# Performance work log

Measured on AMD Instinct MI355X. Metric: run time of the kernel, lower is better.

## Reference

```python
import jax, jax.numpy as jnp
import numpy as np

A = 32           # num_atoms
R = A * (A - 1)  # num_rel (fully connected, no self loops)
B, T, D = 4, 64, 64
S, E = 4, 4      # num_states, edge_types
MH, MO, NH = 256, 256, 256

def _lrelu(x):
    return jax.nn.leaky_relu(x, 0.01)  # torch default slope

def setup_inputs() -> dict:
    key = jax.random.key(0)
    ks = jax.random.split(key, 16)
    # one-hot receiver/sender matrices for a fully connected graph
    off = np.ones((A, A)) - np.eye(A)
    rec_idx, send_idx = np.where(off)
    eye = np.eye(A, dtype=np.float32)
    rel_rec = jnp.asarray(eye[rec_idx])    # [R, A]
    rel_send = jnp.asarray(eye[send_idx])  # [R, A]
    w = 0.05
    return {
        "inputs": jax.random.normal(ks[0], (B, A, T, D), jnp.float32),
        "state": jax.random.uniform(ks[1], (B, A, T, S), jnp.float32),
        "rel_type": jax.random.uniform(ks[2], (B, R, S, E), jnp.float32),
        "rel_rec": rel_rec,
        "rel_send": rel_send,
        "msg_fc1_w": jax.random.normal(ks[3], (E, 2 * D, MH), jnp.float32) * w,
        "msg_fc1_b": jax.random.normal(ks[4], (E, MH), jnp.float32) * w,
        "msg_fc2_w": jax.random.normal(ks[5], (E, MH, MO), jnp.float32) * w,
        "msg_fc2_b": jax.random.normal(ks[6], (E, MO), jnp.float32) * w,
        "out_fc1_w": jax.random.normal(ks[7], (D + MO, NH), jnp.float32) * w,
        "out_fc1_b": jax.random.normal(ks[8], (NH,), jnp.float32) * w,
        "out_fc2_w": jax.random.normal(ks[9], (NH, NH), jnp.float32) * w,
        "out_fc2_b": jax.random.normal(ks[10], (NH,), jnp.float32) * w,
        "out_fc3_w": jax.random.normal(ks[11], (NH, D), jnp.float32) * w,
        "out_fc3_b": jax.random.normal(ks[12], (D,), jnp.float32) * w,
        "pred_steps": 1,
    }

def reference(inputs, state, rel_type, rel_rec, rel_send,
              msg_fc1_w, msg_fc1_b, msg_fc2_w, msg_fc2_b,
              out_fc1_w, out_fc1_b, out_fc2_w, out_fc2_b,
              out_fc3_w, out_fc3_b, pred_steps):
    # hidden_states=True, embedding=False, ball_pos=None, skip_first=True,
    # dropout p=0, pred_steps=1 -> one single_step_forward over all T.
    x = jnp.transpose(inputs, (0, 2, 1, 3))   # [B,T,A,D]
    st = jnp.transpose(state, (0, 2, 1, 3))   # [B,T,A,S]
    t = x.shape[1]

    # gather via one-hot matmuls
    recv = jnp.einsum('ra,btad->btrd', rel_rec, x)    # [B,T,R,D]
    send = jnp.einsum('ra,btad->btrd', rel_send, x)   # [B,T,R,D]
    ss = jnp.einsum('ra,btas->btrs', rel_send, st)    # [B,T,R,S]
    pre_msg = jnp.concatenate([send, recv], axis=-1)  # [B,T,R,2D]

    all_msgs = jnp.zeros(pre_msg.shape[:3] + (MO,), pre_msg.dtype)
    for i in range(1, E):  # skip_first_edge_type
        m = _lrelu(pre_msg @ msg_fc1_w[i] + msg_fc1_b[i])
        m = _lrelu(m @ msg_fc2_w[i] + msg_fc2_b[i])
        # gate: sum over states of rel_type[...,i] * sender states
        g = jnp.einsum('brs,btrs->btr', rel_type[..., i], ss)[..., None]
        all_msgs = all_msgs + m * g

    # scatter-accumulate messages back to receiver nodes
    agg = jnp.einsum('btrm,ra->btam', all_msgs, rel_rec)  # [B,T,A,MO]
    aug = jnp.concatenate([x, agg], axis=-1)              # skip_connection = inputs
    h = _lrelu(aug @ out_fc1_w + out_fc1_b)
    h = _lrelu(h @ out_fc2_w + out_fc2_b)
    pred = h @ out_fc3_w + out_fc3_b
    nxt = x + pred                                        # [B,T,A,D]

    out = nxt[:, : t - 1]                                 # pred_all
    return jnp.transpose(out, (0, 2, 1, 3))               # [B,A,T-1,D]
```

## Files before the change

### kernel.cpp

```cpp
#include <hip/hip_runtime.h>


typedef _Float16 f16x8 __attribute__((ext_vector_type(8)));
typedef float f32x4 __attribute__((ext_vector_type(4)));

#define MFMAH(a, b, c) __builtin_amdgcn_mfma_f32_16x16x32_f16((a), (b), (c), 0, 0, 0)

#define KBAR0() do {                                             \
  __builtin_amdgcn_sched_barrier(0);                             \
  asm volatile("s_waitcnt vmcnt(0) lgkmcnt(0)" ::: "memory");    \
  __builtin_amdgcn_s_barrier();                                  \
  __builtin_amdgcn_sched_barrier(0);                             \
} while (0)

#define KBARL() do {                                             \
  __builtin_amdgcn_sched_barrier(0);                             \
  asm volatile("s_waitcnt lgkmcnt(0)" ::: "memory");             \
  __builtin_amdgcn_s_barrier();                                  \
  __builtin_amdgcn_sched_barrier(0);                             \
} while (0)

__device__ __forceinline__ unsigned pkh(float lo, float hi) {
  auto h = __builtin_amdgcn_cvt_pkrtz(lo, hi);
  return __builtin_bit_cast(unsigned, h);
}
__device__ __forceinline__ unsigned short f2h(float f) {
  return __builtin_bit_cast(unsigned short, (_Float16)f);
}
__device__ __forceinline__ float lrelu(float x) { return x > 0.f ? x : 0.01f * x; }

__device__ __forceinline__ void gl16(const void* g, void* l) {
  __builtin_amdgcn_global_load_lds(
      (const __attribute__((address_space(1))) unsigned int*)(unsigned long long)g,
      (__attribute__((address_space(3))) unsigned int*)(unsigned int)(unsigned long long)l,
      16, 0, 0);
}

__global__ __launch_bounds__(256) void kw(
    const float* __restrict__ w1, const float* __restrict__ w2,
    const float* __restrict__ o1, const float* __restrict__ o2, const float* __restrict__ o3,
    unsigned short* __restrict__ W1T, unsigned short* __restrict__ W2F,
    unsigned short* __restrict__ O1T, unsigned short* __restrict__ O2T,
    unsigned short* __restrict__ O3T) {
  int i = blockIdx.x * 256 + threadIdx.x;
  if (i < 98304) {
    int k = i & 63, n = (i >> 6) & 255, eh = i >> 14;
    int e = (eh >> 1) + 1, half = eh & 1;
    W1T[i] = f2h(w1[(e * 128 + half * 64 + k) * 256 + n]);
    return;
  }
  i -= 98304;
  if (i < 196608) {
    int j = i & 7, l = (i >> 3) & 63, t = (i >> 9) & 15, s = (i >> 13) & 7, e = i >> 16;
    int n = t * 16 + (l & 15);
    int k = s * 32 + (l >> 4) * 8 + j;
    W2F[i] = f2h(w2[(e + 1) * 65536 + k * 256 + n]);
    return;
  }
  i -= 196608;
  if (i < 81920) {
    int k = i % 320, n = i / 320;
    O1T[i] = f2h(o1[k * 256 + n]);
    return;
  }
  i -= 81920;
  if (i < 65536) {
    int k = i & 255, n = i >> 8;
    O2T[i] = f2h(o2[k * 256 + n]);
    return;
  }
  i -= 65536;
  {
    int k = i & 255, n = i >> 8;
    O3T[i] = f2h(o3[k * 64 + n]);
  }
}

__global__ __launch_bounds__(256) void ka(
    const float* __restrict__ inputs, const float* __restrict__ state,
    const float* __restrict__ rel_type, const unsigned short* __restrict__ W1T,
    const float* __restrict__ b1g,
    unsigned short* __restrict__ P, float* __restrict__ G) {
  int t = blockIdx.x, b = blockIdx.y;
  int bt = b * 63 + t;
  int tid = threadIdx.x, lane = tid & 63, wid = tid >> 6;
  int waveM = wid & 1, waveN = wid >> 1;
  __shared__ __align__(16) _Float16 xa[32 * 72];
  __shared__ __align__(16) _Float16 Bt[256 * 72];
  __shared__ __align__(16) _Float16 Ps[32 * 256];
  __shared__ float ss[32][4];
  {
    int a = tid >> 3, d0 = (tid & 7) * 8;
    const float* src = inputs + (((b * 32 + a) * 64 + t) << 6) + d0;
    float4 v0 = *(const float4*)src;
    float4 v1 = *(const float4*)(src + 4);
    uint4 w;
    w.x = pkh(v0.x, v0.y); w.y = pkh(v0.z, v0.w);
    w.z = pkh(v1.x, v1.y); w.w = pkh(v1.z, v1.w);
    *(uint4*)&xa[a * 72 + d0] = w;
  }
  if (tid < 128) {
    int a = tid >> 2, s = tid & 3;
    ss[a][s] = state[((b * 32 + a) * 64 + t) * 4 + s];
  }
  __syncthreads();
  #pragma unroll
  for (int q = 0; q < 12; ++q) {
    int task = tid + q * 256;
    int e = task >> 10, rem = task & 1023, a = rem >> 5, k = rem & 31;
    float g = 0.f;
    if (k < 31) {
      int sA = k + (k >= a ? 1 : 0);
      int r = a * 31 + k;
      const float* rt = rel_type + (b * 992 + r) * 16 + (e + 1);
      g = rt[0] * ss[sA][0] + rt[4] * ss[sA][1] + rt[8] * ss[sA][2] + rt[12] * ss[sA][3];
    }
    G[(bt * 3 + e) * 1024 + a * 32 + k] = g;
  }
  for (int eh = 0; eh < 6; ++eh) {
    #pragma unroll
    for (int q = 0; q < 8; ++q) {
      int cid = tid + q * 256;
      int n = cid >> 3, c8 = (cid & 7) * 8;
      *(uint4*)&Bt[n * 72 + c8] = *(const uint4*)&W1T[(eh * 256 + n) * 64 + c8];
    }
    __syncthreads();
    f32x4 acc[8];
    #pragma unroll
    for (int f = 0; f < 8; ++f) acc[f] = f32x4{0.f, 0.f, 0.f, 0.f};
    #pragma unroll
    for (int ik = 0; ik < 2; ++ik) {
      int k0 = ik * 32;
      f16x8 av = *(const f16x8*)&xa[(waveM * 16 + (lane & 15)) * 72 + k0 + (lane >> 4) * 8];
      #pragma unroll
      for (int f = 0; f < 8; ++f) {
        f16x8 bv = *(const f16x8*)&Bt[(waveN * 128 + f * 16 + (lane & 15)) * 72 + k0 + (lane >> 4) * 8];
        acc[f] = MFMAH(av, bv, acc[f]);
      }
    }
    #pragma unroll
    for (int f = 0; f < 8; ++f) {
      int c = waveN * 128 + f * 16 + (lane & 15);
      float bias = (eh & 1) ? b1g[((eh >> 1) + 1) * 256 + c] : 0.f;
      #pragma unroll
      for (int i = 0; i < 4; ++i) {
        int rrow = waveM * 16 + (lane >> 4) * 4 + i;
        Ps[rrow * 256 + c] = (_Float16)(acc[f][i] + bias);
      }
    }
    __syncthreads();
    unsigned short* dst = P + (bt * 6 + eh) * 8192;
    #pragma unroll
    for (int q = 0; q < 4; ++q) {
      int o = (tid + q * 256) * 8;
      *(uint4*)&dst[o] = *(const uint4*)&Ps[o];
    }
    __syncthreads();
  }
}

__global__ __launch_bounds__(512, 4) void kb(
    const unsigned short* __restrict__ P, const float* __restrict__ G,
    const unsigned short* __restrict__ W2F, const float* __restrict__ b2g,
    unsigned short* __restrict__ AGG3) {
  int bx = blockIdx.x;
  int swz = (bx & 7) * 756 + (bx >> 3);
  int e = swz / 2016;
  int rem = swz - e * 2016;
  int bt = rem >> 3, q = rem & 7;
  int a0 = q * 4;
  int tid = threadIdx.x, lane = tid & 63, wid = tid >> 6;
  int waveM = wid & 1, waveN = wid >> 1;
  int lane15 = lane & 15, kqh = lane >> 4;

  __shared__ __align__(16) _Float16 h1F[2][4096];
  __shared__ __align__(16) _Float16 Bt[3][8192];
  __shared__ float gs[128];
  __shared__ float b2s[256];

  const unsigned short* psrc  = P + (bt * 6 + e * 2) * 8192;
  const unsigned short* prsrc = psrc + 8192;
  const unsigned short* w2f   = W2F + e * 65536;

  int rrow = wid * 16 + lane15;
  int al0 = rrow >> 5, bk = rrow & 31;
  int bs = (bk < 31) ? bk + (bk >= a0 + al0 ? 1 : 0) : 0;
  const unsigned short* pvg = psrc + bs * 256 + kqh * 8;
  const unsigned short* rvg = prsrc + (a0 + al0) * 256 + kqh * 8;
  int h1off = wid * 512 + lane * 8;

  {
    f16x8 pv = *(const f16x8*)(pvg);
    f16x8 rv = *(const f16x8*)(rvg);
    __builtin_amdgcn_sched_barrier(0);
    #pragma unroll
    for (int j = 0; j < 2; ++j) {
      int c = j * 512 + tid;
      gl16(w2f + c * 8, (char*)&Bt[0][0] + c * 16);
      gl16(w2f + 8192 + c * 8, (char*)&Bt[1][0] + c * 16);
    }
    if (tid < 128) gs[tid] = G[((bt * 3 + e) << 10) + a0 * 32 + tid];
    if (tid >= 256) b2s[tid - 256] = b2g[(e + 1) * 256 + (tid - 256)];
    f16x8 h = pv + rv;
    *(f16x8*)&h1F[0][h1off] = __builtin_elementwise_max(h, h * (_Float16)0.01f);
  }
  KBAR0();

  f32x4 acc[4][4];
  #pragma unroll
  for (int f = 0; f < 4; ++f)
    #pragma unroll
    for (int g2 = 0; g2 < 4; ++g2) acc[f][g2] = f32x4{0.f, 0.f, 0.f, 0.f};

  #pragma unroll
  for (int s = 0; s < 8; ++s) {
    const int buf = s & 1;
    f16x8 pv, rv;
    if (s < 7) {
      pv = *(const f16x8*)(pvg + (s + 1) * 32);
      rv = *(const f16x8*)(rvg + (s + 1) * 32);
    }
    __builtin_amdgcn_sched_barrier(0);
    if (s < 6) {
      #pragma unroll
      for (int j = 0; j < 2; ++j) {
        int c = j * 512 + tid;
        gl16(w2f + (s + 2) * 8192 + c * 8, (char*)&Bt[(s + 2) % 3][0] + c * 16);
      }
    }
    f16x8 af[4];
    #pragma unroll
    for (int f = 0; f < 4; ++f)
      af[f] = *(const f16x8*)&h1F[buf][(waveM * 4 + f) * 512 + lane * 8];
    __builtin_amdgcn_s_setprio(1);
    #pragma unroll
    for (int g2 = 0; g2 < 4; ++g2) {
      f16x8 bv = *(const f16x8*)&Bt[s % 3][(waveN * 4 + g2) * 512 + lane * 8];
      #pragma unroll
      for (int f = 0; f < 4; ++f)
        acc[f][g2] = MFMAH(af[f], bv, acc[f][g2]);
    }
    __builtin_amdgcn_s_setprio(0);
    if (s < 7) {
      f16x8 h = pv + rv;
      *(f16x8*)&h1F[buf ^ 1][h1off] = __builtin_elementwise_max(h, h * (_Float16)0.01f);
      if (s < 6)
        asm volatile("s_waitcnt vmcnt(2)" ::: "memory");
      KBARL();
    }
  }

  _Float16* aggh = (_Float16*)AGG3;
  #pragma unroll
  for (int half = 0; half < 2; ++half) {
    int al = waveM * 2 + half;
    #pragma unroll
    for (int g2 = 0; g2 < 4; ++g2) {
      int c = waveN * 64 + g2 * 16 + lane15;
      float bb = b2s[c];
      float p = 0.f;
      #pragma unroll
      for (int fh = 0; fh < 2; ++fh) {
        int f = half * 2 + fh;
        int k4 = fh * 16 + kqh * 4;
        #pragma unroll
        for (int i = 0; i < 4; ++i)
          p += gs[al * 32 + k4 + i] * lrelu(acc[f][g2][i] + bb);
      }
      p += __shfl_xor(p, 16, 64);
      p += __shfl_xor(p, 32, 64);
      if (lane < 16)
        aggh[(size_t)e * 2064384 + (((bt * 32 + a0 + al) << 8) + c)] = (_Float16)p;
    }
  }
}

__global__ __launch_bounds__(256) void kc(
    const float* __restrict__ inputs, const unsigned short* __restrict__ AGG3,
    const unsigned short* __restrict__ O1T, const unsigned short* __restrict__ O2T,
    const unsigned short* __restrict__ O3T,
    const float* __restrict__ ob1, const float* __restrict__ ob2, const float* __restrict__ ob3,
    float* __restrict__ out) {
  int t = blockIdx.x, b = blockIdx.y;
  int bt = b * 63 + t;
  int tid = threadIdx.x, lane = tid & 63, wid = tid >> 6;
  int waveM = wid & 1, waveN = wid >> 1;
  __shared__ __align__(16) _Float16 aug[32 * 328];
  __shared__ __align__(16) _Float16 h1[32 * 264];
  __shared__ __align__(16) _Float16 h2[32 * 264];
  __shared__ __align__(16) _Float16 Bt[256 * 40];
  __shared__ __align__(16) float xs[32 * 64];
  __shared__ float lb1[256], lb2[256], lb3[64];
  {
    int a = tid >> 3, d0 = (tid & 7) * 8;
    const float* src = inputs + (((b * 32 + a) * 64 + t) << 6) + d0;
    float4 v0 = *(const float4*)src;
    float4 v1 = *(const float4*)(src + 4);
    *(float4*)&xs[a * 64 + d0] = v0;
    *(float4*)&xs[a * 64 + d0 + 4] = v1;
    uint4 w;
    w.x = pkh(v0.x, v0.y); w.y = pkh(v0.z, v0.w);
    w.z = pkh(v1.x, v1.y); w.w = pkh(v1.z, v1.w);
    *(uint4*)&aug[a * 328 + d0] = w;
  }
  #pragma unroll
  for (int qq = 0; qq < 4; ++qq) {
    int cid = tid + qq * 256;
    int a = cid >> 5, c8 = (cid & 31) * 8;
    size_t o = ((size_t)(bt * 32 + a) << 8) + c8;
    f16x8 v0 = *(const f16x8*)&AGG3[o];
    f16x8 v1 = *(const f16x8*)&AGG3[2064384 + o];
    f16x8 v2 = *(const f16x8*)&AGG3[4128768 + o];
    f16x8 s = v0 + v1 + v2;
    *(uint4*)&aug[a * 328 + 64 + c8] = __builtin_bit_cast(uint4, s);
  }
  lb1[tid] = ob1[tid];
  lb2[tid] = ob2[tid];
  if (tid < 64) lb3[tid] = ob3[tid];
  __syncthreads();
  f32x4 acc[8];
  #pragma unroll
  for (int f = 0; f < 8; ++f) acc[f] = f32x4{0.f, 0.f, 0.f, 0.f};
  for (int kk = 0; kk < 10; ++kk) {
    #pragma unroll
    for (int q = 0; q < 4; ++q) {
      int cid = tid + q * 256;
      int n = cid >> 2, c8 = (cid & 3) * 8;
      *(uint4*)&Bt[n * 40 + c8] = *(const uint4*)&O1T[n * 320 + kk * 32 + c8];
    }
    __syncthreads();
    f16x8 av = *(const f16x8*)&aug[(waveM * 16 + (lane & 15)) * 328 + kk * 32 + (lane >> 4) * 8];
    #pragma unroll
    for (int f = 0; f < 8; ++f) {
      f16x8 bv = *(const f16x8*)&Bt[(waveN * 128 + f * 16 + (lane & 15)) * 40 + (lane >> 4) * 8];
      acc[f] = MFMAH(av, bv, acc[f]);
    }
    __syncthreads();
  }
  #pragma unroll
  for (int f = 0; f < 8; ++f) {
    int c = waveN * 128 + f * 16 + (lane & 15);
    #pragma unroll
    for (int i = 0; i < 4; ++i) {
      int r = waveM * 16 + (lane >> 4) * 4 + i;
      h1[r * 264 + c] = (_Float16)lrelu(acc[f][i] + lb1[c]);
    }
  }
  __syncthreads();
  #pragma unroll
  for (int f = 0; f < 8; ++f) acc[f] = f32x4{0.f, 0.f, 0.f, 0.f};
  for (int kk = 0; kk < 8; ++kk) {
    #pragma unroll
    for (int q = 0; q < 4; ++q) {
      int cid = tid + q * 256;
      int n = cid >> 2, c8 = (cid & 3) * 8;
      *(uint4*)&Bt[n * 40 + c8] = *(const uint4*)&O2T[n * 256 + kk * 32 + c8];
    }
    __syncthreads();
    f16x8 av = *(const f16x8*)&h1[(waveM * 16 + (lane & 15)) * 264 + kk * 32 + (lane >> 4) * 8];
    #pragma unroll
    for (int f = 0; f < 8; ++f) {
      f16x8 bv = *(const f16x8*)&Bt[(waveN * 128 + f * 16 + (lane & 15)) * 40 + (lane >> 4) * 8];
      acc[f] = MFMAH(av, bv, acc[f]);
    }
    __syncthreads();
  }
  #pragma unroll
  for (int f = 0; f < 8; ++f) {
    int c = waveN * 128 + f * 16 + (lane & 15);
    #pragma unroll
    for (int i = 0; i < 4; ++i) {
      int r = waveM * 16 + (lane >> 4) * 4 + i;
      h2[r * 264 + c] = (_Float16)lrelu(acc[f][i] + lb2[c]);
    }
  }
  __syncthreads();
  f32x4 a3[2];
  a3[0] = f32x4{0.f, 0.f, 0.f, 0.f};
  a3[1] = f32x4{0.f, 0.f, 0.f, 0.f};
  for (int kk = 0; kk < 8; ++kk) {
    {
      int n = tid >> 2, c8 = (tid & 3) * 8;
      *(uint4*)&Bt[n * 40 + c8] = *(const uint4*)&O3T[n * 256 + kk * 32 + c8];
    }
    __syncthreads();
    f16x8 av = *(const f16x8*)&h2[(waveM * 16 + (lane & 15)) * 264 + kk * 32 + (lane >> 4) * 8];
    #pragma unroll
    for (int f = 0; f < 2; ++f) {
      f16x8 bv = *(const f16x8*)&Bt[(waveN * 32 + f * 16 + (lane & 15)) * 40 + (lane >> 4) * 8];
      a3[f] = MFMAH(av, bv, a3[f]);
    }
    __syncthreads();
  }
  #pragma unroll
  for (int f = 0; f < 2; ++f) {
    int d = waveN * 32 + f * 16 + (lane & 15);
    #pragma unroll
    for (int i = 0; i < 4; ++i) {
      int a = waveM * 16 + (lane >> 4) * 4 + i;
      out[((b * 32 + a) * 63 + t) * 64 + d] = a3[f][i] + lb3[d] + xs[a * 64 + d];
    }
  }
}

extern "C" void kernel_launch(void* const* d_in, const int* in_sizes, int n_in,
                              void* d_out, int out_size, void* d_ws, size_t ws_size,
                              hipStream_t stream) {
  const float* inputs   = (const float*)d_in[0];
  const float* state    = (const float*)d_in[1];
  const float* rel_type = (const float*)d_in[2];
  const float* w1  = (const float*)d_in[5];
  const float* b1  = (const float*)d_in[6];
  const float* w2  = (const float*)d_in[7];
  const float* b2  = (const float*)d_in[8];
  const float* o1w = (const float*)d_in[9];
  const float* o1b = (const float*)d_in[10];
  const float* o2w = (const float*)d_in[11];
  const float* o2b = (const float*)d_in[12];
  const float* o3w = (const float*)d_in[13];
  const float* o3b = (const float*)d_in[14];
  char* ws = (char*)d_ws;
  unsigned short* W1T = (unsigned short*)(ws + 0);
  unsigned short* W2F = (unsigned short*)(ws + 196608);
  unsigned short* O1T = (unsigned short*)(ws + 589824);
  unsigned short* O2T = (unsigned short*)(ws + 753664);
  unsigned short* O3T = (unsigned short*)(ws + 884736);
  unsigned short* Pp  = (unsigned short*)(ws + 917504);
  float* G    = (float*)(ws + 25690112);
  unsigned short* AGG3 = (unsigned short*)(ws + 28786688);
  float* out = (float*)d_out;

  kw<<<1792, 256, 0, stream>>>(w1, w2, o1w, o2w, o3w, W1T, W2F, O1T, O2T, O3T);
  ka<<<dim3(63, 4), 256, 0, stream>>>(inputs, state, rel_type, W1T, b1, Pp, G);
  kb<<<6048, 512, 0, stream>>>(Pp, G, W2F, b2, AGG3);
  kc<<<dim3(63, 4), 256, 0, stream>>>(inputs, AGG3, O1T, O2T, O3T, o1b, o2b, o3b, out);
}
```

Measured before the change: 165.0 us.

## Double kb block tile to 256 rows with phased MFMA/load interleaving

Each kb block now handles 8 receiver atoms (256 message rows) instead of 4, halving the grid and the number of times each block streams the W2 tiles through LDS. The K-loop is split into four barrier-separated phases that interleave LDS fragment prefetch, global loads and MFMA groups, with B fragments double-buffered in registers. The aim is to amortize the weight traffic and hide LDS latency. In exchange, accumulator registers double, occupancy drops to 2 blocks per CU, and there are more barriers per step.

```diff
diff --git a/kernel.cpp b/kernel.cpp
--- a/kernel.cpp
+++ b/kernel.cpp
@@ -3,6 +3,7 @@
 
 typedef _Float16 f16x8 __attribute__((ext_vector_type(8)));
 typedef float f32x4 __attribute__((ext_vector_type(4)));
+typedef unsigned short us16;
 
 #define MFMAH(a, b, c) __builtin_amdgcn_mfma_f32_16x16x32_f16((a), (b), (c), 0, 0, 0)
 
@@ -13,9 +14,15 @@
   __builtin_amdgcn_sched_barrier(0);                             \
 } while (0)
 
-#define KBARL() do {                                             \
+#define PH_TOP() do {                                            \
   __builtin_amdgcn_sched_barrier(0);                             \
+  __builtin_amdgcn_s_barrier();                                  \
   asm volatile("s_waitcnt lgkmcnt(0)" ::: "memory");             \
+  __builtin_amdgcn_sched_barrier(0);                             \
+} while (0)
+
+#define PH_END() do {                                            \
+  __builtin_amdgcn_sched_barrier(0);                             \
   __builtin_amdgcn_s_barrier();                                  \
   __builtin_amdgcn_sched_barrier(0);                             \
 } while (0)
@@ -159,118 +166,175 @@
   }
 }
 
-__global__ __launch_bounds__(512, 4) void kb(
+__global__ __launch_bounds__(512, 2) void kb(
     const unsigned short* __restrict__ P, const float* __restrict__ G,
     const unsigned short* __restrict__ W2F, const float* __restrict__ b2g,
     unsigned short* __restrict__ AGG3) {
   int bx = blockIdx.x;
-  int swz = (bx & 7) * 756 + (bx >> 3);
-  int e = swz / 2016;
-  int rem = swz - e * 2016;
-  int bt = rem >> 3, q = rem & 7;
-  int a0 = q * 4;
+  int swz = (bx & 7) * 378 + (bx >> 3);
+  int e = swz / 1008;
+  int rem = swz - e * 1008;
+  int bt = rem >> 2, qq = rem & 3;
   int tid = threadIdx.x, lane = tid & 63, wid = tid >> 6;
   int waveM = wid & 1, waveN = wid >> 1;
   int lane15 = lane & 15, kqh = lane >> 4;
 
-  __shared__ __align__(16) _Float16 h1F[2][4096];
-  __shared__ __align__(16) _Float16 Bt[3][8192];
-  __shared__ float gs[128];
+  __shared__ __align__(16) _Float16 h1F[2][8192];
+  __shared__ __align__(16) _Float16 BtR[3][8192];
+  __shared__ float gs[256];
   __shared__ float b2s[256];
 
   const unsigned short* psrc  = P + (bt * 6 + e * 2) * 8192;
   const unsigned short* prsrc = psrc + 8192;
   const unsigned short* w2f   = W2F + e * 65536;
 
-  int rrow = wid * 16 + lane15;
-  int al0 = rrow >> 5, bk = rrow & 31;
-  int bs = (bk < 31) ? bk + (bk >= a0 + al0 ? 1 : 0) : 0;
-  const unsigned short* pvg = psrc + bs * 256 + kqh * 8;
-  const unsigned short* rvg = prsrc + (a0 + al0) * 256 + kqh * 8;
-  int h1off = wid * 512 + lane * 8;
+  int k1  = (wid & 1) * 16 + lane15;
+  int at1 = qq * 8 + (wid >> 1);
+  int at2 = at1 + 4;
+  int bs1 = (k1 < 31) ? (k1 + (k1 >= at1 ? 1 : 0)) : 0;
+  int bs2 = (k1 < 31) ? (k1 + (k1 >= at2 ? 1 : 0)) : 0;
+  const unsigned short* pv1g = psrc + bs1 * 256 + kqh * 8;
+  const unsigned short* pv2g = psrc + bs2 * 256 + kqh * 8;
+  const unsigned short* rv1g = prsrc + at1 * 256 + kqh * 8;
+  const unsigned short* rv2g = prsrc + at2 * 256 + kqh * 8;
+  int wo1 = tid * 8, wo2 = (tid + 512) * 8;
 
   {
-    f16x8 pv = *(const f16x8*)(pvg);
-    f16x8 rv = *(const f16x8*)(rvg);
+    f16x8 p1 = *(const f16x8*)pv1g;
+    f16x8 p2 = *(const f16x8*)pv2g;
+    f16x8 r1 = *(const f16x8*)rv1g;
+    f16x8 r2 = *(const f16x8*)rv2g;
     __builtin_amdgcn_sched_barrier(0);
     #pragma unroll
     for (int j = 0; j < 2; ++j) {
       int c = j * 512 + tid;
-      gl16(w2f + c * 8, (char*)&Bt[0][0] + c * 16);
-      gl16(w2f + 8192 + c * 8, (char*)&Bt[1][0] + c * 16);
-    }
-    if (tid < 128) gs[tid] = G[((bt * 3 + e) << 10) + a0 * 32 + tid];
-    if (tid >= 256) b2s[tid - 256] = b2g[(e + 1) * 256 + (tid - 256)];
-    f16x8 h = pv + rv;
-    *(f16x8*)&h1F[0][h1off] = __builtin_elementwise_max(h, h * (_Float16)0.01f);
+      gl16(w2f + c * 8, (char*)&BtR[0][0] + c * 16);
+      gl16(w2f + 8192 + c * 8, (char*)&BtR[1][0] + c * 16);
+    }
+    if (tid < 256) gs[tid] = G[((bt * 3 + e) << 10) + qq * 256 + tid];
+    else b2s[tid - 256] = b2g[(e + 1) * 256 + (tid - 256)];
+    f16x8 h = p1 + r1;
+    *(f16x8*)&h1F[0][wo1] = __builtin_elementwise_max(h, h * (_Float16)0.01f);
+    h = p2 + r2;
+    *(f16x8*)&h1F[0][wo2] = __builtin_elementwise_max(h, h * (_Float16)0.01f);
   }
   KBAR0();
 
-  f32x4 acc[4][4];
-  #pragma unroll
-  for (int f = 0; f < 4; ++f)
+  f32x4 acc[8][4];
+  #pragma unroll
+  for (int f = 0; f < 8; ++f)
     #pragma unroll
     for (int g2 = 0; g2 < 4; ++g2) acc[f][g2] = f32x4{0.f, 0.f, 0.f, 0.f};
 
+  f16x8 bvp[2][4], afp[2][2];
+  f16x8 pw1, pw2, rw1, rw2;
+
+  #pragma unroll
+  for (int g2 = 0; g2 < 4; ++g2)
+    bvp[0][g2] = *(const f16x8*)&BtR[0][(waveN * 4 + g2) * 512 + lane * 8];
+  afp[0][0] = *(const f16x8*)&h1F[0][(waveM * 8 + 0) * 512 + lane * 8];
+  afp[0][1] = *(const f16x8*)&h1F[0][(waveM * 8 + 1) * 512 + lane * 8];
+
   #pragma unroll
   for (int s = 0; s < 8; ++s) {
-    const int buf = s & 1;
-    f16x8 pv, rv;
+    const int cb = s & 1, nb = cb ^ 1;
+
+    afp[1][0] = *(const f16x8*)&h1F[cb][(waveM * 8 + 2) * 512 + lane * 8];
+    afp[1][1] = *(const f16x8*)&h1F[cb][(waveM * 8 + 3) * 512 + lane * 8];
     if (s < 7) {
-      pv = *(const f16x8*)(pvg + (s + 1) * 32);
-      rv = *(const f16x8*)(rvg + (s + 1) * 32);
-    }
-    __builtin_amdgcn_sched_barrier(0);
+      pw1 = *(const f16x8*)(pv1g + (s + 1) * 32);
+      pw2 = *(const f16x8*)(pv2g + (s + 1) * 32);
+      rw1 = *(const f16x8*)(rv1g + (s + 1) * 32);
+      rw2 = *(const f16x8*)(rv2g + (s + 1) * 32);
+    }
+    PH_TOP();
+    __builtin_amdgcn_s_setprio(1);
+    #pragma unroll
+    for (int g2 = 0; g2 < 4; ++g2) {
+      acc[0][g2] = MFMAH(afp[0][0], bvp[cb][g2], acc[0][g2]);
+      acc[1][g2] = MFMAH(afp[0][1], bvp[cb][g2], acc[1][g2]);
+    }
+    __builtin_amdgcn_s_setprio(0);
+    PH_END();
+
+    afp[0][0] = *(const f16x8*)&h1F[cb][(waveM * 8 + 4) * 512 + lane * 8];
+    afp[0][1] = *(const f16x8*)&h1F[cb][(waveM * 8 + 5) * 512 + lane * 8];
     if (s < 6) {
       #pragma unroll
       for (int j = 0; j < 2; ++j) {
         int c = j * 512 + tid;
-        gl16(w2f + (s + 2) * 8192 + c * 8, (char*)&Bt[(s + 2) % 3][0] + c * 16);
+        gl16(w2f + (s + 2) * 8192 + c * 8, (char*)&BtR[(s + 2) % 3][0] + c * 16);
       }
     }
-    f16x8 af[4];
-    #pragma unroll
-    for (int f = 0; f < 4; ++f)
-      af[f] = *(const f16x8*)&h1F[buf][(waveM * 4 + f) * 512 + lane * 8];
+    PH_TOP();
     __builtin_amdgcn_s_setprio(1);
     #pragma unroll
     for (int g2 = 0; g2 < 4; ++g2) {
-      f16x8 bv = *(const f16x8*)&Bt[s % 3][(waveN * 4 + g2) * 512 + lane * 8];
+      acc[2][g2] = MFMAH(afp[1][0], bvp[cb][g2], acc[2][g2]);
+      acc[3][g2] = MFMAH(afp[1][1], bvp[cb][g2], acc[3][g2]);
+    }
+    __builtin_amdgcn_s_setprio(0);
+    PH_END();
+
+    afp[1][0] = *(const f16x8*)&h1F[cb][(waveM * 8 + 6) * 512 + lane * 8];
+    afp[1][1] = *(const f16x8*)&h1F[cb][(waveM * 8 + 7) * 512 + lane * 8];
+    if (s < 7) {
+      if (s < 6) asm volatile("s_waitcnt vmcnt(2)" ::: "memory");
+      else       asm volatile("s_waitcnt vmcnt(0)" ::: "memory");
+      f16x8 h = pw1 + rw1;
+      *(f16x8*)&h1F[nb][wo1] = __builtin_elementwise_max(h, h * (_Float16)0.01f);
+      h = pw2 + rw2;
+      *(f16x8*)&h1F[nb][wo2] = __builtin_elementwise_max(h, h * (_Float16)0.01f);
+    }
+    PH_TOP();
+    __builtin_amdgcn_s_setprio(1);
+    #pragma unroll
+    for (int g2 = 0; g2 < 4; ++g2) {
+      acc[4][g2] = MFMAH(afp[0][0], bvp[cb][g2], acc[4][g2]);
+      acc[5][g2] = MFMAH(afp[0][1], bvp[cb][g2], acc[5][g2]);
+    }
+    __builtin_amdgcn_s_setprio(0);
+    PH_END();
+
+    if (s < 7) {
       #pragma unroll
-      for (int f = 0; f < 4; ++f)
-        acc[f][g2] = MFMAH(af[f], bv, acc[f][g2]);
+      for (int g2 = 0; g2 < 4; ++g2)
+        bvp[nb][g2] = *(const f16x8*)&BtR[(s + 1) % 3][(waveN * 4 + g2) * 512 + lane * 8];
+      afp[0][0] = *(const f16x8*)&h1F[nb][(waveM * 8 + 0) * 512 + lane * 8];
+      afp[0][1] = *(const f16x8*)&h1F[nb][(waveM * 8 + 1) * 512 + lane * 8];
+    }
+    PH_TOP();
+    __builtin_amdgcn_s_setprio(1);
+    #pragma unroll
+    for (int g2 = 0; g2 < 4; ++g2) {
+      acc[6][g2] = MFMAH(afp[1][0], bvp[cb][g2], acc[6][g2]);
+      acc[7][g2] = MFMAH(afp[1][1], bvp[cb][g2], acc[7][g2]);
     }
     __builtin_amdgcn_s_setprio(0);
-    if (s < 7) {
-      f16x8 h = pv + rv;
-      *(f16x8*)&h1F[buf ^ 1][h1off] = __builtin_elementwise_max(h, h * (_Float16)0.01f);
-      if (s < 6)
-        asm volatile("s_waitcnt vmcnt(2)" ::: "memory");
-      KBARL();
-    }
+    if (s < 7) PH_END();
   }
 
   _Float16* aggh = (_Float16*)AGG3;
   #pragma unroll
-  for (int half = 0; half < 2; ++half) {
-    int al = waveM * 2 + half;
+  for (int ai = 0; ai < 4; ++ai) {
+    int at = qq * 8 + waveM * 4 + ai;
     #pragma unroll
     for (int g2 = 0; g2 < 4; ++g2) {
-      int c = waveN * 64 + g2 * 16 + lane15;
+      int c = (waveN * 4 + g2) * 16 + lane15;
       float bb = b2s[c];
       float p = 0.f;
       #pragma unroll
-      for (int fh = 0; fh < 2; ++fh) {
-        int f = half * 2 + fh;
-        int k4 = fh * 16 + kqh * 4;
+      for (int half = 0; half < 2; ++half) {
+        int f = ai * 2 + half;
+        int k4 = half * 16 + kqh * 4;
         #pragma unroll
         for (int i = 0; i < 4; ++i)
-          p += gs[al * 32 + k4 + i] * lrelu(acc[f][g2][i] + bb);
+          p += gs[(waveM * 4 + ai) * 32 + k4 + i] * lrelu(acc[f][g2][i] + bb);
       }
       p += __shfl_xor(p, 16, 64);
       p += __shfl_xor(p, 32, 64);
       if (lane < 16)
-        aggh[(size_t)e * 2064384 + (((bt * 32 + a0 + al) << 8) + c)] = (_Float16)p;
+        aggh[(size_t)e * 2064384 + (((bt * 32 + at) << 8) + c)] = (_Float16)p;
     }
   }
 }
@@ -432,6 +496,6 @@
 
   kw<<<1792, 256, 0, stream>>>(w1, w2, o1w, o2w, o3w, W1T, W2F, O1T, O2T, O3T);
   ka<<<dim3(63, 4), 256, 0, stream>>>(inputs, state, rel_type, W1T, b1, Pp, G);
-  kb<<<6048, 512, 0, stream>>>(Pp, G, W2F, b2, AGG3);
+  kb<<<3024, 512, 0, stream>>>(Pp, G, W2F, b2, AGG3);
   kc<<<dim3(63, 4), 256, 0, stream>>>(inputs, AGG3, O1T, O2T, O3T, o1b, o2b, o3b, out);
 }
```

After: 206.7 us. +25.3%, slower.

## Shrink kb tiles to 64 rows and load W2 fragments directly into registers

Applied to the files above, without the earlier changes.

The message-MLP kernel now processes 2 receiver atoms (64 edge rows) per 256-thread block instead of 4 atoms per 512-thread block, doubling the grid. The triple-buffered LDS staging of W2 through global_load_lds is removed, and each wave instead loads its own B fragments straight from global memory into a double-buffered register set. This cuts LDS use and barrier waits, which may raise occupancy. In exchange the W2 weights are re-read from global/L2 twice as often overall, and register pressure rises.

```diff
diff --git a/kernel.cpp b/kernel.cpp
--- a/kernel.cpp
+++ b/kernel.cpp
@@ -28,13 +28,6 @@
   return __builtin_bit_cast(unsigned short, (_Float16)f);
 }
 __device__ __forceinline__ float lrelu(float x) { return x > 0.f ? x : 0.01f * x; }
-
-__device__ __forceinline__ void gl16(const void* g, void* l) {
-  __builtin_amdgcn_global_load_lds(
-      (const __attribute__((address_space(1))) unsigned int*)(unsigned long long)g,
-      (__attribute__((address_space(3))) unsigned int*)(unsigned int)(unsigned long long)l,
-      16, 0, 0);
-}
 
 __global__ __launch_bounds__(256) void kw(
     const float* __restrict__ w1, const float* __restrict__ w2,
@@ -159,48 +152,46 @@
   }
 }
 
-__global__ __launch_bounds__(512, 4) void kb(
+__global__ __launch_bounds__(256, 3) void kb(
     const unsigned short* __restrict__ P, const float* __restrict__ G,
     const unsigned short* __restrict__ W2F, const float* __restrict__ b2g,
     unsigned short* __restrict__ AGG3) {
   int bx = blockIdx.x;
-  int swz = (bx & 7) * 756 + (bx >> 3);
-  int e = swz / 2016;
-  int rem = swz - e * 2016;
-  int bt = rem >> 3, q = rem & 7;
-  int a0 = q * 4;
+  int swz = (bx & 7) * 1512 + (bx >> 3);
+  int e = swz / 4032;
+  int rem = swz - e * 4032;
+  int bt = rem >> 4, q = rem & 15;
   int tid = threadIdx.x, lane = tid & 63, wid = tid >> 6;
-  int waveM = wid & 1, waveN = wid >> 1;
   int lane15 = lane & 15, kqh = lane >> 4;
 
-  __shared__ __align__(16) _Float16 h1F[2][4096];
-  __shared__ __align__(16) _Float16 Bt[3][8192];
-  __shared__ float gs[128];
+  __shared__ __align__(16) _Float16 h1F[2][2048];
+  __shared__ float gs[64];
   __shared__ float b2s[256];
 
   const unsigned short* psrc  = P + (bt * 6 + e * 2) * 8192;
   const unsigned short* prsrc = psrc + 8192;
   const unsigned short* w2f   = W2F + e * 65536;
 
-  int rrow = wid * 16 + lane15;
-  int al0 = rrow >> 5, bk = rrow & 31;
-  int bs = (bk < 31) ? bk + (bk >= a0 + al0 ? 1 : 0) : 0;
+  int r = wid * 16 + lane15;
+  int al0 = r >> 5, bk = r & 31;
+  int aG = q * 2 + al0;
+  int bs = (bk < 31) ? (bk + (bk >= aG ? 1 : 0)) : 0;
   const unsigned short* pvg = psrc + bs * 256 + kqh * 8;
-  const unsigned short* rvg = prsrc + (a0 + al0) * 256 + kqh * 8;
-  int h1off = wid * 512 + lane * 8;
+  const unsigned short* rvg = prsrc + aG * 256 + kqh * 8;
+  int h1off = tid * 8;
+
+  const unsigned short* bvg = w2f + (wid * 4) * 512 + lane * 8;
+
+  f16x8 bvb[2][4];
 
   {
-    f16x8 pv = *(const f16x8*)(pvg);
-    f16x8 rv = *(const f16x8*)(rvg);
-    __builtin_amdgcn_sched_barrier(0);
-    #pragma unroll
-    for (int j = 0; j < 2; ++j) {
-      int c = j * 512 + tid;
-      gl16(w2f + c * 8, (char*)&Bt[0][0] + c * 16);
-      gl16(w2f + 8192 + c * 8, (char*)&Bt[1][0] + c * 16);
-    }
-    if (tid < 128) gs[tid] = G[((bt * 3 + e) << 10) + a0 * 32 + tid];
-    if (tid >= 256) b2s[tid - 256] = b2g[(e + 1) * 256 + (tid - 256)];
+    f16x8 pv = *(const f16x8*)pvg;
+    f16x8 rv = *(const f16x8*)rvg;
+    #pragma unroll
+    for (int g2 = 0; g2 < 4; ++g2)
+      bvb[0][g2] = *(const f16x8*)(bvg + g2 * 512);
+    b2s[tid] = b2g[(e + 1) * 256 + tid];
+    if (tid < 64) gs[tid] = G[((bt * 3 + e) << 10) + q * 64 + tid];
     f16x8 h = pv + rv;
     *(f16x8*)&h1F[0][h1off] = __builtin_elementwise_max(h, h * (_Float16)0.01f);
   }
@@ -214,54 +205,48 @@
 
   #pragma unroll
   for (int s = 0; s < 8; ++s) {
-    const int buf = s & 1;
+    const int cb = s & 1;
     f16x8 pv, rv;
     if (s < 7) {
       pv = *(const f16x8*)(pvg + (s + 1) * 32);
       rv = *(const f16x8*)(rvg + (s + 1) * 32);
     }
     __builtin_amdgcn_sched_barrier(0);
-    if (s < 6) {
+    if (s < 7) {
       #pragma unroll
-      for (int j = 0; j < 2; ++j) {
-        int c = j * 512 + tid;
-        gl16(w2f + (s + 2) * 8192 + c * 8, (char*)&Bt[(s + 2) % 3][0] + c * 16);
-      }
-    }
+      for (int g2 = 0; g2 < 4; ++g2)
+        bvb[cb ^ 1][g2] = *(const f16x8*)(bvg + (s + 1) * 8192 + g2 * 512);
+    }
+    __builtin_amdgcn_sched_barrier(0);
     f16x8 af[4];
     #pragma unroll
     for (int f = 0; f < 4; ++f)
-      af[f] = *(const f16x8*)&h1F[buf][(waveM * 4 + f) * 512 + lane * 8];
+      af[f] = *(const f16x8*)&h1F[cb][f * 512 + lane * 8];
     __builtin_amdgcn_s_setprio(1);
     #pragma unroll
-    for (int g2 = 0; g2 < 4; ++g2) {
-      f16x8 bv = *(const f16x8*)&Bt[s % 3][(waveN * 4 + g2) * 512 + lane * 8];
+    for (int g2 = 0; g2 < 4; ++g2)
       #pragma unroll
       for (int f = 0; f < 4; ++f)
-        acc[f][g2] = MFMAH(af[f], bv, acc[f][g2]);
-    }
+        acc[f][g2] = MFMAH(af[f], bvb[cb][g2], acc[f][g2]);
     __builtin_amdgcn_s_setprio(0);
     if (s < 7) {
       f16x8 h = pv + rv;
-      *(f16x8*)&h1F[buf ^ 1][h1off] = __builtin_elementwise_max(h, h * (_Float16)0.01f);
-      if (s < 6)
-        asm volatile("s_waitcnt vmcnt(2)" ::: "memory");
+      *(f16x8*)&h1F[cb ^ 1][h1off] = __builtin_elementwise_max(h, h * (_Float16)0.01f);
       KBARL();
     }
   }
 
   _Float16* aggh = (_Float16*)AGG3;
   #pragma unroll
-  for (int half = 0; half < 2; ++half) {
-    int al = waveM * 2 + half;
+  for (int al = 0; al < 2; ++al) {
     #pragma unroll
     for (int g2 = 0; g2 < 4; ++g2) {
-      int c = waveN * 64 + g2 * 16 + lane15;
+      int c = wid * 64 + g2 * 16 + lane15;
       float bb = b2s[c];
       float p = 0.f;
       #pragma unroll
       for (int fh = 0; fh < 2; ++fh) {
-        int f = half * 2 + fh;
+        int f = al * 2 + fh;
         int k4 = fh * 16 + kqh * 4;
         #pragma unroll
         for (int i = 0; i < 4; ++i)
@@ -270,7 +255,7 @@
       p += __shfl_xor(p, 16, 64);
       p += __shfl_xor(p, 32, 64);
       if (lane < 16)
-        aggh[(size_t)e * 2064384 + (((bt * 32 + a0 + al) << 8) + c)] = (_Float16)p;
+        aggh[(size_t)e * 2064384 + (((bt * 32 + q * 2 + al) << 8) + c)] = (_Float16)p;
     }
   }
 }
@@ -432,6 +417,6 @@
 
   kw<<<1792, 256, 0, stream>>>(w1, w2, o1w, o2w, o3w, W1T, W2F, O1T, O2T, O3T);
   ka<<<dim3(63, 4), 256, 0, stream>>>(inputs, state, rel_type, W1T, b1, Pp, G);
-  kb<<<6048, 512, 0, stream>>>(Pp, G, W2F, b2, AGG3);
+  kb<<<12096, 256, 0, stream>>>(Pp, G, W2F, b2, AGG3);
   kc<<<dim3(63, 4), 256, 0, stream>>>(inputs, AGG3, O1T, O2T, O3T, o1b, o2b, o3b, out);
 }
```

Result: slower. 173.7 us (+5.3%).
